# Kernel tuning notes

Hardware: AMD Instinct MI355X
Metric: run time of the kernel (lower is better)

Reference implementation:

```python
import jax, jax.numpy as jnp
import numpy as np

B, T, C, D = 16, 4096, 1024, 64  # batch, tokens, d_model, head dim (d_model // n_heads)


def setup_inputs() -> dict:
    key = jax.random.key(0)
    kx, kq, kk, kv = jax.random.split(key, 4)
    scale_w = 1.0 / np.sqrt(C)
    return {
        "x": jax.random.normal(kx, (B, T, C), dtype=jnp.float32),
        "Wq": jax.random.normal(kq, (C, D), dtype=jnp.float32) * scale_w,
        "Wk": jax.random.normal(kk, (C, D), dtype=jnp.float32) * scale_w,
        "Wv": jax.random.normal(kv, (C, D), dtype=jnp.float32) * scale_w,
    }


def reference(x, Wq, Wk, Wv):
    # q, k, v: [B, T, D]; bias-free linear projections
    q = jnp.einsum("btc,cd->btd", x, Wq)
    k = jnp.einsum("btc,cd->btd", x, Wk)
    v = jnp.einsum("btc,cd->btd", x, Wv)
    # scores scaled by C**-0.5 (full d_model, matching the original module)
    scale = jnp.asarray(C, x.dtype) ** -0.5
    wei = jnp.einsum("bqd,bkd->bqk", q, k) * scale  # [B, T, T]
    wei = jax.nn.softmax(wei, axis=-1)
    # dropout is identity in eval mode
    return jnp.einsum("bqk,bkd->bqd", wei, v)  # [B, T, D]
```

## Files before the change

kernel.cpp:

```cpp
#include <hip/hip_runtime.h>
#include <stdint.h>

#define B_ 16
#define T_ 4096
#define C_ 1024
#define D_ 64
#define LOG2E 1.4426950408889634f

using f32x4 = __attribute__((ext_vector_type(4))) float;
using f32x16 = __attribute__((ext_vector_type(16))) float;
using bf16x8 = __attribute__((ext_vector_type(8))) short;
union U8 { uint32_t u[4]; bf16x8 v; };

__device__ __forceinline__ unsigned short f2bf(float x) {
  union { float f; uint32_t u; } v; v.f = x;
  uint32_t r = (v.u + 0x7fffu + ((v.u >> 16) & 1u)) >> 16;
  return (unsigned short)r;
}

__device__ __forceinline__ uint32_t cvtpk(float lo, float hi) {
  uint32_t r;
  asm("v_cvt_pk_bf16_f32 %0, %1, %2" : "=v"(r) : "v"(lo), "v"(hi));
  return r;
}

__device__ __forceinline__ void plswap(uint32_t& a, uint32_t& b) {
  asm volatile("v_permlane32_swap_b32 %0, %1" : "+v"(a), "+v"(b));
}

__device__ __forceinline__ void gload16(const void* gptr, void* lptr) {
  auto g = (const __attribute__((address_space(1))) uint32_t*)(uintptr_t)gptr;
  auto l = (__attribute__((address_space(3))) uint32_t*)(uintptr_t)lptr;
  __builtin_amdgcn_global_load_lds(g, l, 16, 0, 0);
}

#define SYNC_VM0()  asm volatile("s_waitcnt vmcnt(0)\ns_barrier" ::: "memory")

__global__ void k_prep(const float* __restrict__ Wq, const float* __restrict__ Wk,
                       const float* __restrict__ Wv, unsigned short* __restrict__ Wt) {
  int idx = blockIdx.x * 256 + threadIdx.x;
  int n = idx >> 10, k = idx & 1023;
  const float* W = (n < 64) ? Wq : (n < 128 ? Wk : Wv);
  Wt[idx] = f2bf(W[(size_t)k * 64 + (n & 63)]);
}

__global__ __launch_bounds__(256) void k_proj(const float* __restrict__ X,
                                              const unsigned short* __restrict__ Wt,
                                              unsigned short* __restrict__ Qo,
                                              unsigned short* __restrict__ Ko,
                                              unsigned short* __restrict__ Vto) {
  __shared__ float Xs[128 * 32];
  __shared__ unsigned short Ws[192 * 32];
  const int tid = threadIdx.x;
  const int wave = tid >> 6, lane = tid & 63;
  const int g = lane >> 4, c = lane & 15;
  const int m0 = blockIdx.x * 128;

  f32x4 acc[2][12];
#pragma unroll
  for (int a = 0; a < 2; ++a)
#pragma unroll
    for (int b2 = 0; b2 < 12; ++b2) acc[a][b2] = f32x4{0.f, 0.f, 0.f, 0.f};

  const int xrow = tid >> 3, xseg = tid & 7;
  const int wrow = tid >> 2, wseg = tid & 3;

  for (int step = 0; step < 32; ++step) {
    const int k0 = step * 32;
#pragma unroll
    for (int p = 0; p < 4; ++p) {
      int row = p * 32 + xrow;
      int seg = xseg ^ (row & 7);
      gload16(X + (size_t)(m0 + row) * C_ + k0 + seg * 4,
              (char*)Xs + p * 4096 + wave * 1024);
    }
#pragma unroll
    for (int p = 0; p < 3; ++p) {
      int n = p * 64 + wrow;
      int seg = wseg ^ ((n >> 1) & 3);
      gload16(Wt + (size_t)n * C_ + k0 + seg * 8,
              (char*)Ws + p * 4096 + wave * 1024);
    }
    __syncthreads();

    bf16x8 af[2];
#pragma unroll
    for (int mi = 0; mi < 2; ++mi) {
      int row = wave * 32 + mi * 16 + c;
      int sub = g * 2;
      f32x4 x0 = *(const f32x4*)((const char*)Xs + row * 128 + (((sub) ^ (row & 7)) * 16));
      f32x4 x1 = *(const f32x4*)((const char*)Xs + row * 128 + (((sub + 1) ^ (row & 7)) * 16));
      bf16x8 t;
      t[0] = (short)f2bf(x0[0]); t[1] = (short)f2bf(x0[1]);
      t[2] = (short)f2bf(x0[2]); t[3] = (short)f2bf(x0[3]);
      t[4] = (short)f2bf(x1[0]); t[5] = (short)f2bf(x1[1]);
      t[6] = (short)f2bf(x1[2]); t[7] = (short)f2bf(x1[3]);
      af[mi] = t;
    }
#pragma unroll
    for (int ni = 0; ni < 12; ++ni) {
      int n = ni * 16 + c;
      bf16x8 bf = *(const bf16x8*)((const char*)Ws + n * 64 + ((g ^ ((n >> 1) & 3)) * 16));
      acc[0][ni] = __builtin_amdgcn_mfma_f32_16x16x32_bf16(af[0], bf, acc[0][ni], 0, 0, 0);
      acc[1][ni] = __builtin_amdgcn_mfma_f32_16x16x32_bf16(af[1], bf, acc[1][ni], 0, 0, 0);
    }
    __syncthreads();
  }

  const int b = m0 >> 12;
#pragma unroll
  for (int mi = 0; mi < 2; ++mi) {
    int r0 = m0 + wave * 32 + mi * 16 + g * 4;
#pragma unroll
    for (int ni = 0; ni < 12; ++ni) {
      int col = ni * 16 + c;
      if (ni < 4) {
#pragma unroll
        for (int i = 0; i < 4; ++i)
          Qo[(size_t)(r0 + i) * D_ + col] = f2bf(acc[mi][ni][i] * (0.03125f * LOG2E));
      } else if (ni < 8) {
        int d = col - 64;
#pragma unroll
        for (int i = 0; i < 4; ++i)
          Ko[(size_t)(r0 + i) * D_ + d] = f2bf(acc[mi][ni][i]);
      } else {
        int d = col - 128;
        int tt = r0 & (T_ - 1);
        ushort4 pk;
        pk.x = f2bf(acc[mi][ni][0]); pk.y = f2bf(acc[mi][ni][1]);
        pk.z = f2bf(acc[mi][ni][2]); pk.w = f2bf(acc[mi][ni][3]);
        *(ushort4*)(Vto + (size_t)b * (D_ * T_) + (size_t)d * T_ + tt) = pk;
      }
    }
  }
}

__global__ __launch_bounds__(256, 3) void k_attn(const unsigned short* __restrict__ Qi,
                                                 const unsigned short* __restrict__ Ki,
                                                 const unsigned short* __restrict__ Vti,
                                                 float* __restrict__ Out) {
  __shared__ char LDSBUF[6 * 8192];

  const int tid = threadIdx.x;
  const int wave = tid >> 6, lane = tid & 63;
  const int ql = lane & 31;
  const int hi = lane >> 5;
  const int b = blockIdx.y;
  const int qb = blockIdx.x * 128 + wave * 32;

  const unsigned short* Qb = Qi + (size_t)b * T_ * D_;
  const unsigned short* Kb = Ki + (size_t)b * T_ * D_;
  const unsigned short* Vb = Vti + (size_t)b * D_ * T_;

  bf16x8 qf[4];
#pragma unroll
  for (int ks = 0; ks < 4; ++ks)
    qf[ks] = *(const bf16x8*)(Qb + (size_t)(qb + ql) * D_ + ks * 16 + 8 * hi);

  f32x16 o0, o1;
  float l_loc = 0.f;
#pragma unroll
  for (int i = 0; i < 16; ++i) { o0[i] = 0.f; o1[i] = 0.f; }

  const int srow = tid >> 3, sseg = tid & 7;

#define STAGE(BUF, KT)                                                          \
  do {                                                                          \
    char* kb_ = LDSBUF + (BUF) * 8192 + wave * 1024;                            \
    char* vb_ = LDSBUF + 24576 + (BUF) * 8192 + wave * 1024;                    \
    _Pragma("unroll") for (int p = 0; p < 2; ++p) {                             \
      int row = p * 32 + srow;                                                  \
      int seg = sseg ^ (row & 7);                                               \
      gload16(Kb + (size_t)((KT) * 64 + row) * D_ + seg * 8, kb_ + p * 4096);   \
      gload16(Vb + (size_t)row * T_ + (KT) * 64 + seg * 8, vb_ + p * 4096);     \
    }                                                                           \
  } while (0)

#define PACK_TB(SC, PB_EVEN, PB_ODD)                                            \
  do {                                                                          \
    float p_[16];                                                               \
    _Pragma("unroll") for (int r = 0; r < 16; ++r)                              \
        p_[r] = __builtin_amdgcn_exp2f((SC)[r]);                                \
    float a0 = (p_[0] + p_[1]) + (p_[2] + p_[3]);                               \
    float a1 = (p_[4] + p_[5]) + (p_[6] + p_[7]);                               \
    float a2 = (p_[8] + p_[9]) + (p_[10] + p_[11]);                             \
    float a3 = (p_[12] + p_[13]) + (p_[14] + p_[15]);                           \
    l_loc += (a0 + a1) + (a2 + a3);                                             \
    uint32_t w00 = cvtpk(p_[0], p_[1]),   w01 = cvtpk(p_[2], p_[3]);            \
    uint32_t w10 = cvtpk(p_[4], p_[5]),   w11 = cvtpk(p_[6], p_[7]);            \
    uint32_t w20 = cvtpk(p_[8], p_[9]),   w21 = cvtpk(p_[10], p_[11]);          \
    uint32_t w30 = cvtpk(p_[12], p_[13]), w31 = cvtpk(p_[14], p_[15]);          \
    plswap(w00, w10); plswap(w01, w11);                                         \
    plswap(w20, w30); plswap(w21, w31);                                         \
    { U8 t_; t_.u[0] = w00; t_.u[1] = w01; t_.u[2] = w10; t_.u[3] = w11;        \
      PB_EVEN = t_.v; }                                                         \
    { U8 t_; t_.u[0] = w20; t_.u[1] = w21; t_.u[2] = w30; t_.u[3] = w31;        \
      PB_ODD = t_.v; }                                                          \
  } while (0)

#define TILE_COMPUTE(BUF)                                                       \
  do {                                                                          \
    const char* kb_ = LDSBUF + (BUF) * 8192;                                    \
    const char* vb_ = LDSBUF + 24576 + (BUF) * 8192;                            \
    f32x16 s0, s1;                                                              \
    _Pragma("unroll") for (int i = 0; i < 16; ++i) { s0[i] = 0.f; s1[i] = 0.f; }\
    __builtin_amdgcn_s_setprio(1);                                              \
    _Pragma("unroll") for (int ks = 0; ks < 4; ++ks) {                          \
      int sg = ((2 * ks + hi) ^ (ql & 7)) * 16;                                 \
      bf16x8 kf0 = *(const bf16x8*)(kb_ + ql * 128 + sg);                       \
      bf16x8 kf1 = *(const bf16x8*)(kb_ + (32 + ql) * 128 + sg);                \
      s0 = __builtin_amdgcn_mfma_f32_32x32x16_bf16(kf0, qf[ks], s0, 0, 0, 0);   \
      s1 = __builtin_amdgcn_mfma_f32_32x32x16_bf16(kf1, qf[ks], s1, 0, 0, 0);   \
    }                                                                           \
    __builtin_amdgcn_s_setprio(0);                                              \
    bf16x8 pb[4];                                                               \
    PACK_TB(s0, pb[0], pb[1]);                                                  \
    PACK_TB(s1, pb[2], pb[3]);                                                  \
    __builtin_amdgcn_s_setprio(1);                                              \
    _Pragma("unroll") for (int s = 0; s < 4; ++s) {                             \
      int sg = ((2 * s + hi) ^ (ql & 7)) * 16;                                  \
      bf16x8 vf0 = *(const bf16x8*)(vb_ + ql * 128 + sg);                       \
      bf16x8 vf1 = *(const bf16x8*)(vb_ + (32 + ql) * 128 + sg);                \
      o0 = __builtin_amdgcn_mfma_f32_32x32x16_bf16(vf0, pb[s], o0, 0, 0, 0);    \
      o1 = __builtin_amdgcn_mfma_f32_32x32x16_bf16(vf1, pb[s], o1, 0, 0, 0);    \
    }                                                                           \
    __builtin_amdgcn_s_setprio(0);                                              \
  } while (0)

  STAGE(0, 0);
  STAGE(1, 1);
  int cur = 0;
  for (int kt = 0; kt < 62; ++kt) {
    SYNC_VM0();
    int nxt = cur + 2; if (nxt >= 3) nxt -= 3;
    STAGE(nxt, kt + 2);
    TILE_COMPUTE(cur);
    ++cur; if (cur == 3) cur = 0;
  }
  SYNC_VM0();
  TILE_COMPUTE(cur);
  SYNC_VM0();
  TILE_COMPUTE(0);

  float l_tot = l_loc + __shfl_xor(l_loc, 32);
  float inv = 1.0f / l_tot;
  float* Ob = Out + ((size_t)b * T_ + qb + ql) * D_;
#pragma unroll
  for (int rq = 0; rq < 4; ++rq) {
    f32x4 t0, t1;
#pragma unroll
    for (int i = 0; i < 4; ++i) { t0[i] = o0[4 * rq + i] * inv; t1[i] = o1[4 * rq + i] * inv; }
    *(f32x4*)(Ob + rq * 8 + hi * 4) = t0;
    *(f32x4*)(Ob + 32 + rq * 8 + hi * 4) = t1;
  }
#undef STAGE
#undef PACK_TB
#undef TILE_COMPUTE
}

extern "C" void kernel_launch(void* const* d_in, const int* in_sizes, int n_in,
                              void* d_out, int out_size, void* d_ws, size_t ws_size,
                              hipStream_t stream) {
  const float* x  = (const float*)d_in[0];
  const float* Wq = (const float*)d_in[1];
  const float* Wk = (const float*)d_in[2];
  const float* Wv = (const float*)d_in[3];
  float* out = (float*)d_out;
  char* ws = (char*)d_ws;
  unsigned short* Wt = (unsigned short*)(ws);
  unsigned short* Qb = (unsigned short*)(ws + (1u << 20));
  unsigned short* Kb = (unsigned short*)(ws + (9u << 20));
  unsigned short* Vt = (unsigned short*)(ws + (17u << 20));

  k_prep<<<768, 256, 0, stream>>>(Wq, Wk, Wv, Wt);
  k_proj<<<512, 256, 0, stream>>>(x, Wt, Qb, Kb, Vt);
  k_attn<<<dim3(T_ / 128, B_), 256, 0, stream>>>(Qb, Kb, Vt, out);
}
```

Measured before the change: 156.7 us.

## Split key tile across wave pairs, each wave handling 64 queries, merge in LDS

Each block's four waves now form two pairs. Each pair shares 64 queries, and within a pair each wave processes half of every 64-key tile. Each K fragment feeds two MFMAs (one per query group), which halves LDS K reads per MFMA, and each V fragment likewise feeds two MFMAs. Partial outputs and row sums from the second wave of each pair are reduced through LDS at the end. Register pressure roughly doubles for accumulators, so launch bounds drop from 3 to 2 blocks per CU, which risks lower occupancy and less latency hiding.

```diff
diff --git a/kernel.cpp b/kernel.cpp
--- a/kernel.cpp
+++ b/kernel.cpp
@@ -34,7 +34,9 @@
   __builtin_amdgcn_global_load_lds(g, l, 16, 0, 0);
 }
 
-#define SYNC_VM0()  asm volatile("s_waitcnt vmcnt(0)\ns_barrier" ::: "memory")
+#define SYNC_VM0()      asm volatile("s_waitcnt vmcnt(0)\ns_barrier" ::: "memory")
+#define SYNC_VM0_LGKM() asm volatile("s_waitcnt vmcnt(0) lgkmcnt(0)\ns_barrier" ::: "memory")
+#define SYNC_LGKM()     asm volatile("s_waitcnt lgkmcnt(0)\ns_barrier" ::: "memory")
 
 __global__ void k_prep(const float* __restrict__ Wq, const float* __restrict__ Wk,
                        const float* __restrict__ Wv, unsigned short* __restrict__ Wt) {
@@ -135,7 +137,7 @@
   }
 }
 
-__global__ __launch_bounds__(256, 3) void k_attn(const unsigned short* __restrict__ Qi,
+__global__ __launch_bounds__(256, 2) void k_attn(const unsigned short* __restrict__ Qi,
                                                  const unsigned short* __restrict__ Ki,
                                                  const unsigned short* __restrict__ Vti,
                                                  float* __restrict__ Out) {
@@ -145,22 +147,26 @@
   const int wave = tid >> 6, lane = tid & 63;
   const int ql = lane & 31;
   const int hi = lane >> 5;
+  const int qsel = wave & 1;
+  const int th = wave >> 1;
   const int b = blockIdx.y;
-  const int qb = blockIdx.x * 128 + wave * 32;
+  const int qb = blockIdx.x * 128 + qsel * 64;
 
   const unsigned short* Qb = Qi + (size_t)b * T_ * D_;
   const unsigned short* Kb = Ki + (size_t)b * T_ * D_;
   const unsigned short* Vb = Vti + (size_t)b * D_ * T_;
 
-  bf16x8 qf[4];
-#pragma unroll
-  for (int ks = 0; ks < 4; ++ks)
-    qf[ks] = *(const bf16x8*)(Qb + (size_t)(qb + ql) * D_ + ks * 16 + 8 * hi);
-
-  f32x16 o0, o1;
-  float l_loc = 0.f;
-#pragma unroll
-  for (int i = 0; i < 16; ++i) { o0[i] = 0.f; o1[i] = 0.f; }
+  bf16x8 qf[2][4];
+#pragma unroll
+  for (int qg = 0; qg < 2; ++qg)
+#pragma unroll
+    for (int ks = 0; ks < 4; ++ks)
+      qf[qg][ks] = *(const bf16x8*)(Qb + (size_t)(qb + qg * 32 + ql) * D_ + ks * 16 + 8 * hi);
+
+  f32x16 o00, o01, o10, o11;
+  float l_loc0 = 0.f, l_loc1 = 0.f;
+#pragma unroll
+  for (int i = 0; i < 16; ++i) { o00[i] = 0.f; o01[i] = 0.f; o10[i] = 0.f; o11[i] = 0.f; }
 
   const int srow = tid >> 3, sseg = tid & 7;
 
@@ -176,7 +182,7 @@
     }                                                                           \
   } while (0)
 
-#define PACK_TB(SC, PB_EVEN, PB_ODD)                                            \
+#define PACK_TB(SC, LREF, PB0, PB1)                                             \
   do {                                                                          \
     float p_[16];                                                               \
     _Pragma("unroll") for (int r = 0; r < 16; ++r)                              \
@@ -185,7 +191,7 @@
     float a1 = (p_[4] + p_[5]) + (p_[6] + p_[7]);                               \
     float a2 = (p_[8] + p_[9]) + (p_[10] + p_[11]);                             \
     float a3 = (p_[12] + p_[13]) + (p_[14] + p_[15]);                           \
-    l_loc += (a0 + a1) + (a2 + a3);                                             \
+    LREF += (a0 + a1) + (a2 + a3);                                              \
     uint32_t w00 = cvtpk(p_[0], p_[1]),   w01 = cvtpk(p_[2], p_[3]);            \
     uint32_t w10 = cvtpk(p_[4], p_[5]),   w11 = cvtpk(p_[6], p_[7]);            \
     uint32_t w20 = cvtpk(p_[8], p_[9]),   w21 = cvtpk(p_[10], p_[11]);          \
@@ -193,9 +199,9 @@
     plswap(w00, w10); plswap(w01, w11);                                         \
     plswap(w20, w30); plswap(w21, w31);                                         \
     { U8 t_; t_.u[0] = w00; t_.u[1] = w01; t_.u[2] = w10; t_.u[3] = w11;        \
-      PB_EVEN = t_.v; }                                                         \
+      PB0 = t_.v; }                                                             \
     { U8 t_; t_.u[0] = w20; t_.u[1] = w21; t_.u[2] = w30; t_.u[3] = w31;        \
-      PB_ODD = t_.v; }                                                          \
+      PB1 = t_.v; }                                                             \
   } while (0)
 
 #define TILE_COMPUTE(BUF)                                                       \
@@ -207,22 +213,25 @@
     __builtin_amdgcn_s_setprio(1);                                              \
     _Pragma("unroll") for (int ks = 0; ks < 4; ++ks) {                          \
       int sg = ((2 * ks + hi) ^ (ql & 7)) * 16;                                 \
-      bf16x8 kf0 = *(const bf16x8*)(kb_ + ql * 128 + sg);                       \
-      bf16x8 kf1 = *(const bf16x8*)(kb_ + (32 + ql) * 128 + sg);                \
-      s0 = __builtin_amdgcn_mfma_f32_32x32x16_bf16(kf0, qf[ks], s0, 0, 0, 0);   \
-      s1 = __builtin_amdgcn_mfma_f32_32x32x16_bf16(kf1, qf[ks], s1, 0, 0, 0);   \
+      bf16x8 kf = *(const bf16x8*)(kb_ + (th * 32 + ql) * 128 + sg);            \
+      s0 = __builtin_amdgcn_mfma_f32_32x32x16_bf16(kf, qf[0][ks], s0, 0, 0, 0); \
+      s1 = __builtin_amdgcn_mfma_f32_32x32x16_bf16(kf, qf[1][ks], s1, 0, 0, 0); \
     }                                                                           \
     __builtin_amdgcn_s_setprio(0);                                              \
-    bf16x8 pb[4];                                                               \
-    PACK_TB(s0, pb[0], pb[1]);                                                  \
-    PACK_TB(s1, pb[2], pb[3]);                                                  \
+    bf16x8 pb00, pb01, pb10, pb11;                                              \
+    PACK_TB(s0, l_loc0, pb00, pb01);                                            \
+    PACK_TB(s1, l_loc1, pb10, pb11);                                            \
     __builtin_amdgcn_s_setprio(1);                                              \
-    _Pragma("unroll") for (int s = 0; s < 4; ++s) {                             \
-      int sg = ((2 * s + hi) ^ (ql & 7)) * 16;                                  \
-      bf16x8 vf0 = *(const bf16x8*)(vb_ + ql * 128 + sg);                       \
-      bf16x8 vf1 = *(const bf16x8*)(vb_ + (32 + ql) * 128 + sg);                \
-      o0 = __builtin_amdgcn_mfma_f32_32x32x16_bf16(vf0, pb[s], o0, 0, 0, 0);    \
-      o1 = __builtin_amdgcn_mfma_f32_32x32x16_bf16(vf1, pb[s], o1, 0, 0, 0);    \
+    _Pragma("unroll") for (int ts = 0; ts < 2; ++ts) {                          \
+      bf16x8 pb0_ = ts ? pb01 : pb00;                                           \
+      bf16x8 pb1_ = ts ? pb11 : pb10;                                           \
+      int sgv = ((4 * th + 2 * ts + hi) ^ (ql & 7)) * 16;                       \
+      bf16x8 vf0 = *(const bf16x8*)(vb_ + ql * 128 + sgv);                      \
+      bf16x8 vf1 = *(const bf16x8*)(vb_ + (32 + ql) * 128 + sgv);               \
+      o00 = __builtin_amdgcn_mfma_f32_32x32x16_bf16(vf0, pb0_, o00, 0, 0, 0);   \
+      o10 = __builtin_amdgcn_mfma_f32_32x32x16_bf16(vf0, pb1_, o10, 0, 0, 0);   \
+      o01 = __builtin_amdgcn_mfma_f32_32x32x16_bf16(vf1, pb0_, o01, 0, 0, 0);   \
+      o11 = __builtin_amdgcn_mfma_f32_32x32x16_bf16(vf1, pb1_, o11, 0, 0, 0);   \
     }                                                                           \
     __builtin_amdgcn_s_setprio(0);                                              \
   } while (0)
@@ -242,16 +251,50 @@
   SYNC_VM0();
   TILE_COMPUTE(0);
 
-  float l_tot = l_loc + __shfl_xor(l_loc, 32);
-  float inv = 1.0f / l_tot;
-  float* Ob = Out + ((size_t)b * T_ + qb + ql) * D_;
-#pragma unroll
-  for (int rq = 0; rq < 4; ++rq) {
-    f32x4 t0, t1;
-#pragma unroll
-    for (int i = 0; i < 4; ++i) { t0[i] = o0[4 * rq + i] * inv; t1[i] = o1[4 * rq + i] * inv; }
-    *(f32x4*)(Ob + rq * 8 + hi * 4) = t0;
-    *(f32x4*)(Ob + 32 + rq * 8 + hi * 4) = t1;
+  float l0 = l_loc0 + __shfl_xor(l_loc0, 32);
+  float l1 = l_loc1 + __shfl_xor(l_loc1, 32);
+
+  SYNC_VM0_LGKM();
+  if (wave >= 2) {
+    char* mo = LDSBUF + qsel * 20480 + lane * 256;
+#pragma unroll
+    for (int rq = 0; rq < 4; ++rq) {
+      *(f32x4*)(mo + rq * 16)       = f32x4{o00[4*rq], o00[4*rq+1], o00[4*rq+2], o00[4*rq+3]};
+      *(f32x4*)(mo + 64 + rq * 16)  = f32x4{o01[4*rq], o01[4*rq+1], o01[4*rq+2], o01[4*rq+3]};
+      *(f32x4*)(mo + 128 + rq * 16) = f32x4{o10[4*rq], o10[4*rq+1], o10[4*rq+2], o10[4*rq+3]};
+      *(f32x4*)(mo + 192 + rq * 16) = f32x4{o11[4*rq], o11[4*rq+1], o11[4*rq+2], o11[4*rq+3]};
+    }
+    *(float*)(LDSBUF + 44032 + qsel * 512 + lane * 8)     = l0;
+    *(float*)(LDSBUF + 44032 + qsel * 512 + lane * 8 + 4) = l1;
+  }
+  SYNC_LGKM();
+  if (wave < 2) {
+    const char* mo = LDSBUF + qsel * 20480 + lane * 256;
+    float lp0 = *(const float*)(LDSBUF + 44032 + qsel * 512 + lane * 8);
+    float lp1 = *(const float*)(LDSBUF + 44032 + qsel * 512 + lane * 8 + 4);
+    float inv0 = 1.0f / (l0 + lp0);
+    float inv1 = 1.0f / (l1 + lp1);
+    float* Ob0 = Out + ((size_t)b * T_ + qb + ql) * D_;
+    float* Ob1 = Out + ((size_t)b * T_ + qb + 32 + ql) * D_;
+#pragma unroll
+    for (int rq = 0; rq < 4; ++rq) {
+      f32x4 p0 = *(const f32x4*)(mo + rq * 16);
+      f32x4 p1 = *(const f32x4*)(mo + 64 + rq * 16);
+      f32x4 p2 = *(const f32x4*)(mo + 128 + rq * 16);
+      f32x4 p3 = *(const f32x4*)(mo + 192 + rq * 16);
+      f32x4 t0, t1, t2, t3;
+#pragma unroll
+      for (int i = 0; i < 4; ++i) {
+        t0[i] = (o00[4*rq+i] + p0[i]) * inv0;
+        t1[i] = (o01[4*rq+i] + p1[i]) * inv0;
+        t2[i] = (o10[4*rq+i] + p2[i]) * inv1;
+        t3[i] = (o11[4*rq+i] + p3[i]) * inv1;
+      }
+      *(f32x4*)(Ob0 + rq * 8 + hi * 4)      = t0;
+      *(f32x4*)(Ob0 + 32 + rq * 8 + hi * 4) = t1;
+      *(f32x4*)(Ob1 + rq * 8 + hi * 4)      = t2;
+      *(f32x4*)(Ob1 + 32 + rq * 8 + hi * 4) = t3;
+    }
   }
 #undef STAGE
 #undef PACK_TB
```

Measured after the change: 154.1 us, median of 2. Within noise of the previous version (-1.7%).
